# Performance work log

Measured on AMD Instinct MI355X. Metric: run time of the kernel, lower is better.

Reference implementation:

```python
import jax, jax.numpy as jnp
import numpy as np

B, C, H, W = 8, 512, 64, 64
NUMS, V_C = 1024, 512
RATE = 0.999


def _normalize(x):
    # matches torch F.normalize(dim=-1, eps=1e-12)
    return x / jnp.clip(jnp.linalg.norm(x, axis=-1, keepdims=True), 1e-12)


def setup_inputs() -> dict:
    key = jax.random.key(0)
    k1, k2, k3 = jax.random.split(key, 3)
    return {
        "x": jax.random.normal(k1, (B, C, H, W), dtype=jnp.float32),
        "noise_feature": jax.random.normal(k2, (NUMS, C), dtype=jnp.float32),
        "std": jax.random.normal(k3, (NUMS, V_C), dtype=jnp.float32),
    }


def reference(x, noise_feature, std):
    b, c, h, w = x.shape
    # (b,c,h,w) -> (n,c)
    xf = jnp.transpose(x, (0, 2, 3, 1)).reshape(-1, c)
    m = jax.lax.stop_gradient(noise_feature)  # torch uses .data (no grad)
    xn = _normalize(xf)
    mn = _normalize(m)
    score = xn @ mn.T  # (n, k) cosine similarities

    # EMA codebook update (training path, update_flag=True)
    xd = jax.lax.stop_gradient(xf)
    embed_ind = jnp.argmax(score, axis=1)  # (n,)
    # segment_sum == x.T @ one_hot(ind), transposed; avoids dense one-hot GEMM
    embed_sum = jax.ops.segment_sum(xd, embed_ind, num_segments=NUMS)  # (k, c)
    counts = jax.ops.segment_sum(jnp.ones((xd.shape[0],), xd.dtype), embed_ind,
                                 num_segments=NUMS)  # (k,)
    embed_mean = embed_sum / (counts[:, None] + 1e-6)
    new_m = m * RATE + embed_mean * (1.0 - RATE)

    mn2 = _normalize(new_m)
    score2 = xn @ mn2.T  # (n, k)
    soft_label = jax.nn.softmax(score2, axis=1)
    out = (soft_label @ std).reshape(b, h, w, V_C)
    return out, score2
```

## Files before the change

kernel.cpp:

```cpp
#include <hip/hip_runtime.h>
#include <stdint.h>

#define NROWS 32768
#define CDIM  512
#define KCODES 1024
#define VC    512

typedef unsigned short u16;
typedef unsigned long long u64;
using bf16x8 = __attribute__((ext_vector_type(8))) __bf16;
using f32x4  = __attribute__((ext_vector_type(4))) float;

__device__ __forceinline__ float bf2f(u16 u){
  union { unsigned int i; float f; } x; x.i = ((unsigned int)u) << 16; return x.f;
}
__device__ __forceinline__ u16 f2bf(float f){
  union { float f; unsigned int i; } x; x.f = f;
  unsigned int u = x.i;
  u += 0x7fffu + ((u >> 16) & 1u);
  return (u16)(u >> 16);
}
__device__ __forceinline__ unsigned int pack2(u16 lo, u16 hi){
  return (unsigned int)lo | ((unsigned int)hi << 16);
}
__device__ __forceinline__ unsigned int fkey(float f){
  unsigned int u = __float_as_uint(f);
  return (u & 0x80000000u) ? ~u : (u | 0x80000000u);
}
__device__ __forceinline__ f32x4 mfma16(bf16x8 a, bf16x8 b, f32x4 c){
  return __builtin_amdgcn_mfma_f32_16x16x32_bf16(a, b, c, 0, 0, 0);
}
__device__ __forceinline__ void gload_lds16(const void* g, void* l){
  __builtin_amdgcn_global_load_lds(
      (const __attribute__((address_space(1))) unsigned int*)g,
      (__attribute__((address_space(3))) unsigned int*)l, 16, 0, 0);
}

__global__ __launch_bounds__(256) void k_transpose_x(const float* __restrict__ x,
                                                     u16* __restrict__ xf){
  __shared__ float tile[32][33];
  int b  = blockIdx.z;
  int p0 = blockIdx.x * 32;
  int c0 = blockIdx.y * 32;
  int tx = threadIdx.x, ty = threadIdx.y;
  const float* xb = x + (size_t)b * CDIM * 4096;
#pragma unroll
  for (int i = 0; i < 4; i++){
    int c = c0 + ty + i * 8;
    tile[ty + i * 8][tx] = xb[(size_t)c * 4096 + p0 + tx];
  }
  __syncthreads();
#pragma unroll
  for (int i = 0; i < 4; i++){
    int p = p0 + ty + i * 8;
    xf[((size_t)(b * 4096 + p)) * CDIM + c0 + tx] = f2bf(tile[tx][ty + i * 8]);
  }
}

__global__ __launch_bounds__(256) void k_rownorm(const u16* __restrict__ xf,
                                                 float* __restrict__ rinv){
  int row  = blockIdx.x * 4 + (threadIdx.x >> 6);
  int lane = threadIdx.x & 63;
  const uint4* p = (const uint4*)(xf + (size_t)row * CDIM);
  uint4 v = p[lane];
  unsigned int w[4] = {v.x, v.y, v.z, v.w};
  float s = 0.f;
#pragma unroll
  for (int i = 0; i < 4; i++){
    float a = bf2f((u16)(w[i] & 0xffffu));
    float b = bf2f((u16)(w[i] >> 16));
    s += a * a + b * b;
  }
#pragma unroll
  for (int off = 32; off; off >>= 1) s += __shfl_xor(s, off, 64);
  if (lane == 0) rinv[row] = 1.0f / fmaxf(sqrtf(s), 1e-12f);
}

__global__ __launch_bounds__(256) void k_norm_rows(const float* __restrict__ in,
                                                   u16* __restrict__ out){
  int row  = blockIdx.x * 4 + (threadIdx.x >> 6);
  int lane = threadIdx.x & 63;
  const float* r = in + (size_t)row * CDIM;
  float v[8]; float s = 0.f;
#pragma unroll
  for (int i = 0; i < 8; i++){ v[i] = r[lane + i * 64]; s += v[i] * v[i]; }
#pragma unroll
  for (int off = 32; off; off >>= 1) s += __shfl_xor(s, off, 64);
  float inv = 1.0f / fmaxf(sqrtf(s), 1e-12f);
#pragma unroll
  for (int i = 0; i < 8; i++) out[(size_t)row * CDIM + lane + i * 64] = f2bf(v[i] * inv);
}

__global__ __launch_bounds__(256) void k_transpose_std(const float* __restrict__ sd,
                                                       u16* __restrict__ stdT){
  __shared__ float tile[32][33];
  int k0 = blockIdx.x * 32;
  int v0 = blockIdx.y * 32;
  int tx = threadIdx.x, ty = threadIdx.y;
#pragma unroll
  for (int i = 0; i < 4; i++)
    tile[ty + i * 8][tx] = sd[(size_t)(k0 + ty + i * 8) * VC + v0 + tx];
  __syncthreads();
#pragma unroll
  for (int i = 0; i < 4; i++)
    stdT[(size_t)(v0 + ty + i * 8) * KCODES + k0 + tx] = f2bf(tile[tx][ty + i * 8]);
}

__global__ __launch_bounds__(256) void k_gemm1_am(const u16* __restrict__ xf,
                                                  const u16* __restrict__ mn,
                                                  u64* __restrict__ packed){
  __shared__ u16 As[128 * 64];
  __shared__ u16 Bs[128 * 64];
  int tid  = threadIdx.x;
  int wave = tid >> 6, lane = tid & 63;
  int wr = wave >> 1, wc = wave & 1;
  int quad = lane >> 4, l15 = lane & 15;
  int c0 = blockIdx.x * 128, r0 = blockIdx.y * 128;

  int srow = lane >> 3, schunk = lane & 7;
  const u16* ag = xf + (size_t)(r0 + wave * 8 + srow) * CDIM + schunk * 8;
  const u16* bg = mn + (size_t)(c0 + wave * 8 + srow) * CDIM + schunk * 8;
  u16* adst = As + wave * 8 * 64;
  u16* bdst = Bs + wave * 8 * 64;

  f32x4 acc[4][4];
#pragma unroll
  for (int rt = 0; rt < 4; rt++)
#pragma unroll
    for (int ct = 0; ct < 4; ct++) acc[rt][ct] = (f32x4)(0.f);

  for (int k0 = 0; k0 < CDIM; k0 += 64){
#pragma unroll
    for (int i = 0; i < 4; i++){
      gload_lds16(ag + (size_t)i * 32 * CDIM + k0, adst + i * 32 * 64);
      gload_lds16(bg + (size_t)i * 32 * CDIM + k0, bdst + i * 32 * 64);
    }
    __syncthreads();
#pragma unroll
    for (int ks = 0; ks < 2; ks++){
      bf16x8 af[4], bfr[4];
#pragma unroll
      for (int rt = 0; rt < 4; rt++)
        af[rt] = *(const bf16x8*)(As + (wr * 64 + rt * 16 + l15) * 64 + ks * 32 + quad * 8);
#pragma unroll
      for (int ct = 0; ct < 4; ct++)
        bfr[ct] = *(const bf16x8*)(Bs + (wc * 64 + ct * 16 + l15) * 64 + ks * 32 + quad * 8);
#pragma unroll
      for (int rt = 0; rt < 4; rt++)
#pragma unroll
        for (int ct = 0; ct < 4; ct++)
          acc[rt][ct] = mfma16(af[rt], bfr[ct], acc[rt][ct]);
    }
    __syncthreads();
  }

#pragma unroll
  for (int rt = 0; rt < 4; rt++){
#pragma unroll
    for (int q = 0; q < 4; q++){
      float bv = acc[rt][0][q];
      int   bc = c0 + wc * 64 + l15;
#pragma unroll
      for (int ct = 1; ct < 4; ct++){
        float v = acc[rt][ct][q];
        int   c = c0 + wc * 64 + ct * 16 + l15;
        if (v > bv){ bv = v; bc = c; }
      }
#pragma unroll
      for (int off = 1; off <= 8; off <<= 1){
        float ov = __shfl_xor(bv, off, 64);
        int   oc = __shfl_xor(bc, off, 64);
        if (ov > bv || (ov == bv && oc < bc)){ bv = ov; bc = oc; }
      }
      if (l15 == 0){
        int rg = r0 + wr * 64 + rt * 16 + quad * 4 + q;
        u64 key = ((u64)fkey(bv) << 32) | (unsigned int)(~(unsigned int)bc);
        atomicMax(packed + rg, key);
      }
    }
  }
}

__global__ __launch_bounds__(256) void k_decode(const u64* __restrict__ packed,
                                                int* __restrict__ ind){
  int i = blockIdx.x * 256 + threadIdx.x;
  ind[i] = (int)(~(unsigned int)(packed[i] & 0xffffffffull)) & (KCODES - 1);
}

__global__ __launch_bounds__(256) void k_gather(const int* __restrict__ ind,
                                                const u16* __restrict__ xf,
                                                float* __restrict__ esum,
                                                float* __restrict__ counts){
  __shared__ float part[4][CDIM];
  __shared__ int   wcnt[4];
  int code = blockIdx.x;
  int tid = threadIdx.x, wave = tid >> 6, lane = tid & 63;
  float acc[8] = {0,0,0,0,0,0,0,0};
  int cnt = 0;
  for (int base = wave * 64; base < NROWS; base += 256){
    int match = (ind[base + lane] == code);
    u64 mask = __ballot(match);
    cnt += (int)__popcll(mask);
    while (mask){
      int b = __ffsll((long long)mask) - 1;
      mask &= mask - 1;
      int rr = base + b;
      uint4 v = *(const uint4*)(xf + (size_t)rr * CDIM + lane * 8);
      unsigned int w[4] = {v.x, v.y, v.z, v.w};
#pragma unroll
      for (int i = 0; i < 4; i++){
        acc[2 * i]     += bf2f((u16)(w[i] & 0xffffu));
        acc[2 * i + 1] += bf2f((u16)(w[i] >> 16));
      }
    }
  }
#pragma unroll
  for (int j = 0; j < 8; j++) part[wave][lane * 8 + j] = acc[j];
  if (lane == 0) wcnt[wave] = cnt;
  __syncthreads();
  for (int c = tid; c < CDIM; c += 256)
    esum[(size_t)code * CDIM + c] = part[0][c] + part[1][c] + part[2][c] + part[3][c];
  if (tid == 0) counts[code] = (float)(wcnt[0] + wcnt[1] + wcnt[2] + wcnt[3]);
}

__global__ __launch_bounds__(256) void k_newm(const float* __restrict__ m,
                                              const float* __restrict__ esum,
                                              const float* __restrict__ counts,
                                              u16* __restrict__ mn2){
  int row  = blockIdx.x * 4 + (threadIdx.x >> 6);
  int lane = threadIdx.x & 63;
  float cnt = counts[row];
  float sc  = 0.001f / (cnt + 1e-6f);
  float v[8]; float s = 0.f;
#pragma unroll
  for (int i = 0; i < 8; i++){
    int c = lane + i * 64;
    v[i] = m[(size_t)row * CDIM + c] * 0.999f + esum[(size_t)row * CDIM + c] * sc;
    s += v[i] * v[i];
  }
#pragma unroll
  for (int off = 32; off; off >>= 1) s += __shfl_xor(s, off, 64);
  float inv = 1.0f / fmaxf(sqrtf(s), 1e-12f);
#pragma unroll
  for (int i = 0; i < 8; i++) mn2[(size_t)row * CDIM + lane + i * 64] = f2bf(v[i] * inv);
}

#define SM_AS   0
#define SM_BS   65536
#define SM_VS   98304
#define SM_SF   131072
#define SM_PT   140288
#define SM_RM   144384
#define SM_RL   144640
#define SM_RS   144896
__global__ __launch_bounds__(512) void k_fused(const u16* __restrict__ xf,
                                               const u16* __restrict__ mn2,
                                               const float* __restrict__ rinv,
                                               const u16* __restrict__ stdT,
                                               float* __restrict__ score2,
                                               float* __restrict__ out){
  __shared__ char smem[145152];
  char* AsB = smem + SM_AS;
  char* BsB = smem + SM_BS;
  char* VsB = smem + SM_VS;
  float* Sf = (float*)(smem + SM_SF);
  char* PtB = smem + SM_PT;
  float* rowm = (float*)(smem + SM_RM);
  float* rowl = (float*)(smem + SM_RL);
  float* rowsc = (float*)(smem + SM_RS);

  int tid  = threadIdx.x;
  int wave = tid >> 6, lane = tid & 63;
  int quad = lane >> 4, l15 = lane & 15;
  int r0 = blockIdx.x * 64;

  int fr = wave >> 1, fc = wave & 1;
  int ar = fr * 16 + l15;
  int br = fc * 16 + l15;

  int wr2 = wave >> 2, wc4 = wave & 3;
  int R = wr2 * 32, C = wc4 * 128;

  int srow = tid >> 3, ssub = tid & 7;
  float rv = rinv[r0 + srow];

  f32x4 acc[2][8];
#pragma unroll
  for (int rt = 0; rt < 2; rt++)
#pragma unroll
    for (int ct = 0; ct < 8; ct++) acc[rt][ct] = (f32x4)(0.f);

#pragma unroll
  for (int i = 0; i < 8; i++){
    int rr = wave * 8 + i;
    gload_lds16(xf + (size_t)(r0 + rr) * CDIM + ((lane ^ (rr & 7)) * 8),
                AsB + rr * 1024);
  }
#pragma unroll
  for (int i = 0; i < 4; i++){
    int rr = wave + i * 8;
    gload_lds16(mn2 + (size_t)rr * CDIM + ((lane ^ (rr & 7)) * 8),
                BsB + rr * 1024);
  }
#pragma unroll
  for (int i = 0; i < 4; i++){
    int vb = (wave * 4 + i) * 16;
    int vc = vb + (lane >> 2);
    gload_lds16(stdT + (size_t)vc * KCODES + (((lane & 3) ^ (vc & 3)) * 8),
                VsB + vb * 64);
  }
  if (tid < 64){ rowm[tid] = -3.0e38f; rowl[tid] = 0.f; }
  asm volatile("s_waitcnt vmcnt(0)" ::: "memory");
  __syncthreads();

  for (int t = 0; t < 32; ++t){
    int kt = t * 32;
    f32x4 sacc = (f32x4)(0.f);
#pragma unroll
    for (int ks = 0; ks < 16; ++ks){
      bf16x8 a = *(const bf16x8*)(AsB + ar * 1024 + (((ks * 4 + quad) ^ (ar & 7)) << 4));
      bf16x8 b = *(const bf16x8*)(BsB + br * 1024 + (((ks * 4 + quad) ^ (br & 7)) << 4));
      sacc = mfma16(a, b, sacc);
    }
#pragma unroll
    for (int q = 0; q < 4; ++q)
      Sf[(fr * 16 + quad * 4 + q) * 36 + fc * 16 + l15] = sacc[q];
    asm volatile("s_waitcnt lgkmcnt(0)" ::: "memory");
    __builtin_amdgcn_s_barrier();
    if (t + 1 < 32){
#pragma unroll
      for (int i = 0; i < 4; i++){
        int rr = wave + i * 8;
        gload_lds16(mn2 + (size_t)(kt + 32 + rr) * CDIM + ((lane ^ (rr & 7)) * 8),
                    BsB + rr * 1024);
      }
    }
    {
      f32x4 v = *(const f32x4*)(Sf + srow * 36 + ssub * 4);
      v *= rv;
      *(f32x4*)(score2 + (size_t)(r0 + srow) * KCODES + kt + ssub * 4) = v;
      float mx = fmaxf(fmaxf(v[0], v[1]), fmaxf(v[2], v[3]));
      mx = fmaxf(mx, __shfl_xor(mx, 1, 64));
      mx = fmaxf(mx, __shfl_xor(mx, 2, 64));
      mx = fmaxf(mx, __shfl_xor(mx, 4, 64));
      float mo = rowm[srow];
      float mn_ = fmaxf(mo, mx);
      float d = __expf(mo - mn_);
      float p0 = __expf(v[0] - mn_), p1 = __expf(v[1] - mn_);
      float p2 = __expf(v[2] - mn_), p3 = __expf(v[3] - mn_);
      float ss = p0 + p1 + p2 + p3;
      ss += __shfl_xor(ss, 1, 64);
      ss += __shfl_xor(ss, 2, 64);
      ss += __shfl_xor(ss, 4, 64);
      if (ssub == 0){
        rowl[srow] = rowl[srow] * d + ss;
        rowm[srow] = mn_;
        rowsc[srow] = d;
      }
      uint2 pw;
      pw.x = pack2(f2bf(p0), f2bf(p1));
      pw.y = pack2(f2bf(p2), f2bf(p3));
      *(uint2*)(PtB + srow * 64 + (((ssub >> 1) ^ (srow & 3)) << 4) + ((ssub & 1) << 3)) = pw;
    }
    asm volatile("s_waitcnt vmcnt(4) lgkmcnt(0)" ::: "memory");
    __builtin_amdgcn_s_barrier();
    __builtin_amdgcn_sched_barrier(0);
#pragma unroll
    for (int rt = 0; rt < 2; rt++)
#pragma unroll
      for (int q = 0; q < 4; q++){
        float s = rowsc[R + rt * 16 + quad * 4 + q];
#pragma unroll
        for (int ct = 0; ct < 8; ct++) acc[rt][ct][q] *= s;
      }
    bf16x8 pa[2];
#pragma unroll
    for (int rt = 0; rt < 2; rt++){
      int rr = R + rt * 16 + l15;
      pa[rt] = *(const bf16x8*)(PtB + rr * 64 + ((quad ^ (rr & 3)) << 4));
    }
#pragma unroll
    for (int ct = 0; ct < 8; ct++){
      int vc = C + ct * 16 + l15;
      bf16x8 bv = *(const bf16x8*)(VsB + vc * 64 + ((quad ^ (vc & 3)) << 4));
#pragma unroll
      for (int rt = 0; rt < 2; rt++) acc[rt][ct] = mfma16(pa[rt], bv, acc[rt][ct]);
    }
    asm volatile("s_waitcnt lgkmcnt(0)" ::: "memory");
    __builtin_amdgcn_s_barrier();
    if (t + 1 < 32){
#pragma unroll
      for (int i = 0; i < 4; i++){
        int vb = (wave * 4 + i) * 16;
        int vc = vb + (lane >> 2);
        gload_lds16(stdT + (size_t)vc * KCODES + kt + 32 + (((lane & 3) ^ (vc & 3)) * 8),
                    VsB + vb * 64);
      }
      asm volatile("s_waitcnt vmcnt(4)" ::: "memory");
      __builtin_amdgcn_s_barrier();
      __builtin_amdgcn_sched_barrier(0);
    }
  }

#pragma unroll
  for (int rt = 0; rt < 2; rt++)
#pragma unroll
    for (int q = 0; q < 4; q++){
      int rr = R + rt * 16 + quad * 4 + q;
      float inv = 1.0f / rowl[rr];
#pragma unroll
      for (int ct = 0; ct < 8; ct++)
        out[(size_t)(r0 + rr) * VC + C + ct * 16 + l15] = acc[rt][ct][q] * inv;
    }
}

extern "C" void kernel_launch(void* const* d_in, const int* in_sizes, int n_in,
                              void* d_out, int out_size, void* d_ws, size_t ws_size,
                              hipStream_t stream){
  (void)in_sizes; (void)n_in; (void)out_size; (void)ws_size;
  const float* x      = (const float*)d_in[0];
  const float* m      = (const float*)d_in[1];
  const float* stdmat = (const float*)d_in[2];
  float* out    = (float*)d_out;
  float* score2 = out + (size_t)NROWS * VC;

  char* ws = (char*)d_ws;
  u16*   xf     = (u16*)  (ws + 0);
  u16*   mn     = (u16*)  (ws + 33554432);
  u16*   mn2    = (u16*)  (ws + 34603008);
  u16*   stdT   = (u16*)  (ws + 35651584);
  float* rinv   = (float*)(ws + 36700160);
  u64*   packed = (u64*)  (ws + 36831232);
  int*   ind    = (int*)  (ws + 37093376);
  float* esum   = (float*)(ws + 37224448);
  float* counts = (float*)(ws + 39321600);

  hipMemsetAsync(packed, 0, (size_t)NROWS * 8, stream);

  k_transpose_x  <<<dim3(128, 16, 8), dim3(32, 8), 0, stream>>>(x, xf);
  k_rownorm      <<<NROWS / 4, 256, 0, stream>>>(xf, rinv);
  k_norm_rows    <<<KCODES / 4, 256, 0, stream>>>(m, mn);
  k_transpose_std<<<dim3(32, 16), dim3(32, 8), 0, stream>>>(stdmat, stdT);
  k_gemm1_am     <<<dim3(KCODES / 128, NROWS / 128), 256, 0, stream>>>(xf, mn, packed);
  k_decode       <<<NROWS / 256, 256, 0, stream>>>(packed, ind);
  k_gather       <<<KCODES, 256, 0, stream>>>(ind, xf, esum, counts);
  k_newm         <<<KCODES / 4, 256, 0, stream>>>(m, esum, counts, mn2);
  k_fused        <<<NROWS / 64, 512, 0, stream>>>(xf, mn2, rinv, stdT, score2, out);
}
```

Measured before the change: 541.3 us.

## Enlarge code tile in fused softmax kernel and load std fragments directly

The fused score/softmax/output kernel now processes 64 codes per tile instead of 32, halving the number of online-softmax iterations and barriers. The std matrix is no longer staged through LDS; each wave reads its bf16 fragments straight from global memory into registers. Separately, the decode kernel is removed and the gather kernel decodes the packed argmax keys itself, saving one launch and an intermediate buffer. Direct global reads of std may expose memory latency that the earlier LDS prefetch hid, and the larger register footprint could lower occupancy.

```diff
diff --git a/kernel.cpp b/kernel.cpp
--- a/kernel.cpp
+++ b/kernel.cpp
@@ -109,8 +109,8 @@
 __global__ __launch_bounds__(256) void k_gemm1_am(const u16* __restrict__ xf,
                                                   const u16* __restrict__ mn,
                                                   u64* __restrict__ packed){
-  __shared__ u16 As[128 * 64];
-  __shared__ u16 Bs[128 * 64];
+  __shared__ __align__(16) u16 As[128 * 64];
+  __shared__ __align__(16) u16 Bs[128 * 64];
   int tid  = threadIdx.x;
   int wave = tid >> 6, lane = tid & 63;
   int wr = wave >> 1, wc = wave & 1;
@@ -181,13 +181,7 @@
   }
 }
 
-__global__ __launch_bounds__(256) void k_decode(const u64* __restrict__ packed,
-                                                int* __restrict__ ind){
-  int i = blockIdx.x * 256 + threadIdx.x;
-  ind[i] = (int)(~(unsigned int)(packed[i] & 0xffffffffull)) & (KCODES - 1);
-}
-
-__global__ __launch_bounds__(256) void k_gather(const int* __restrict__ ind,
+__global__ __launch_bounds__(256) void k_gather(const u64* __restrict__ packed,
                                                 const u16* __restrict__ xf,
                                                 float* __restrict__ esum,
                                                 float* __restrict__ counts){
@@ -198,7 +192,9 @@
   float acc[8] = {0,0,0,0,0,0,0,0};
   int cnt = 0;
   for (int base = wave * 64; base < NROWS; base += 256){
-    int match = (ind[base + lane] == code);
+    u64 pk = packed[base + lane];
+    int cl = (int)(~(unsigned int)(pk & 0xffffffffull)) & (KCODES - 1);
+    int match = (cl == code);
     u64 mask = __ballot(match);
     cnt += (int)__popcll(mask);
     while (mask){
@@ -245,41 +241,32 @@
   for (int i = 0; i < 8; i++) mn2[(size_t)row * CDIM + lane + i * 64] = f2bf(v[i] * inv);
 }
 
-#define SM_AS   0
-#define SM_BS   65536
-#define SM_VS   98304
-#define SM_SF   131072
-#define SM_PT   140288
-#define SM_RM   144384
-#define SM_RL   144640
-#define SM_RS   144896
+#define NTILE 16
+#define TCODE 64
 __global__ __launch_bounds__(512) void k_fused(const u16* __restrict__ xf,
                                                const u16* __restrict__ mn2,
                                                const float* __restrict__ rinv,
                                                const u16* __restrict__ stdT,
                                                float* __restrict__ score2,
                                                float* __restrict__ out){
-  __shared__ char smem[145152];
-  char* AsB = smem + SM_AS;
-  char* BsB = smem + SM_BS;
-  char* VsB = smem + SM_VS;
-  float* Sf = (float*)(smem + SM_SF);
-  char* PtB = smem + SM_PT;
-  float* rowm = (float*)(smem + SM_RM);
-  float* rowl = (float*)(smem + SM_RL);
-  float* rowsc = (float*)(smem + SM_RS);
+  __shared__ __align__(16) u16 As[64 * 512];
+  __shared__ __align__(16) u16 Bs[64 * 512];
+  __shared__ __align__(16) float Sf[64 * 68];
+  __shared__ __align__(16) u16 Pt[64 * 72];
+  __shared__ float rowm[64], rowl[64], rowsc[64];
 
   int tid  = threadIdx.x;
   int wave = tid >> 6, lane = tid & 63;
   int quad = lane >> 4, l15 = lane & 15;
   int r0 = blockIdx.x * 64;
 
-  int fr = wave >> 1, fc = wave & 1;
-  int ar = fr * 16 + l15;
-  int br = fc * 16 + l15;
-
-  int wr2 = wave >> 2, wc4 = wave & 3;
-  int R = wr2 * 32, C = wc4 * 128;
+  int sR = (wave >> 2) * 32;
+  int sC = (wave & 3) * 16;
+  int ar0 = sR + l15, ar1 = sR + 16 + l15;
+  int br  = sC + l15;
+
+  int R2 = (wave >> 2) * 32;
+  int C2 = (wave & 3) * 128;
 
   int srow = tid >> 3, ssub = tid & 7;
   float rv = rinv[r0 + srow];
@@ -294,61 +281,61 @@
   for (int i = 0; i < 8; i++){
     int rr = wave * 8 + i;
     gload_lds16(xf + (size_t)(r0 + rr) * CDIM + ((lane ^ (rr & 7)) * 8),
-                AsB + rr * 1024);
-  }
-#pragma unroll
-  for (int i = 0; i < 4; i++){
-    int rr = wave + i * 8;
+                As + rr * 512);
     gload_lds16(mn2 + (size_t)rr * CDIM + ((lane ^ (rr & 7)) * 8),
-                BsB + rr * 1024);
-  }
-#pragma unroll
-  for (int i = 0; i < 4; i++){
-    int vb = (wave * 4 + i) * 16;
-    int vc = vb + (lane >> 2);
-    gload_lds16(stdT + (size_t)vc * KCODES + (((lane & 3) ^ (vc & 3)) * 8),
-                VsB + vb * 64);
+                Bs + rr * 512);
   }
   if (tid < 64){ rowm[tid] = -3.0e38f; rowl[tid] = 0.f; }
   asm volatile("s_waitcnt vmcnt(0)" ::: "memory");
-  __syncthreads();
-
-  for (int t = 0; t < 32; ++t){
-    int kt = t * 32;
-    f32x4 sacc = (f32x4)(0.f);
+  __builtin_amdgcn_s_barrier();
+
+  for (int t = 0; t < NTILE; ++t){
+    int kt = t * TCODE;
+    f32x4 s0 = (f32x4)(0.f), s1 = (f32x4)(0.f);
 #pragma unroll
     for (int ks = 0; ks < 16; ++ks){
-      bf16x8 a = *(const bf16x8*)(AsB + ar * 1024 + (((ks * 4 + quad) ^ (ar & 7)) << 4));
-      bf16x8 b = *(const bf16x8*)(BsB + br * 1024 + (((ks * 4 + quad) ^ (br & 7)) << 4));
-      sacc = mfma16(a, b, sacc);
-    }
-#pragma unroll
-    for (int q = 0; q < 4; ++q)
-      Sf[(fr * 16 + quad * 4 + q) * 36 + fc * 16 + l15] = sacc[q];
+      bf16x8 b  = *(const bf16x8*)(Bs + br * 512 + (((ks * 4 + quad) ^ (br & 7)) << 3));
+      bf16x8 a0 = *(const bf16x8*)(As + ar0 * 512 + (((ks * 4 + quad) ^ (ar0 & 7)) << 3));
+      bf16x8 a1 = *(const bf16x8*)(As + ar1 * 512 + (((ks * 4 + quad) ^ (ar1 & 7)) << 3));
+      s0 = mfma16(a0, b, s0);
+      s1 = mfma16(a1, b, s1);
+    }
+#pragma unroll
+    for (int q = 0; q < 4; ++q){
+      Sf[(sR + quad * 4 + q) * 68 + sC + l15]      = s0[q];
+      Sf[(sR + 16 + quad * 4 + q) * 68 + sC + l15] = s1[q];
+    }
     asm volatile("s_waitcnt lgkmcnt(0)" ::: "memory");
     __builtin_amdgcn_s_barrier();
-    if (t + 1 < 32){
-#pragma unroll
-      for (int i = 0; i < 4; i++){
-        int rr = wave + i * 8;
-        gload_lds16(mn2 + (size_t)(kt + 32 + rr) * CDIM + ((lane ^ (rr & 7)) * 8),
-                    BsB + rr * 1024);
+    if (t + 1 < NTILE){
+#pragma unroll
+      for (int i = 0; i < 8; i++){
+        int rr = wave * 8 + i;
+        gload_lds16(mn2 + (size_t)(kt + TCODE + rr) * CDIM + ((lane ^ (rr & 7)) * 8),
+                    Bs + rr * 512);
       }
     }
     {
-      f32x4 v = *(const f32x4*)(Sf + srow * 36 + ssub * 4);
-      v *= rv;
-      *(f32x4*)(score2 + (size_t)(r0 + srow) * KCODES + kt + ssub * 4) = v;
-      float mx = fmaxf(fmaxf(v[0], v[1]), fmaxf(v[2], v[3]));
+      f32x4 u = *(const f32x4*)(Sf + srow * 68 + ssub * 8);
+      f32x4 w = *(const f32x4*)(Sf + srow * 68 + ssub * 8 + 4);
+      u *= rv; w *= rv;
+      float* so = score2 + (size_t)(r0 + srow) * KCODES + kt + ssub * 8;
+      *(f32x4*)(so)     = u;
+      *(f32x4*)(so + 4) = w;
+      float mx = fmaxf(fmaxf(fmaxf(u[0], u[1]), fmaxf(u[2], u[3])),
+                       fmaxf(fmaxf(w[0], w[1]), fmaxf(w[2], w[3])));
       mx = fmaxf(mx, __shfl_xor(mx, 1, 64));
       mx = fmaxf(mx, __shfl_xor(mx, 2, 64));
       mx = fmaxf(mx, __shfl_xor(mx, 4, 64));
       float mo = rowm[srow];
       float mn_ = fmaxf(mo, mx);
       float d = __expf(mo - mn_);
-      float p0 = __expf(v[0] - mn_), p1 = __expf(v[1] - mn_);
-      float p2 = __expf(v[2] - mn_), p3 = __expf(v[3] - mn_);
-      float ss = p0 + p1 + p2 + p3;
+      float p[8];
+#pragma unroll
+      for (int j = 0; j < 4; j++){ p[j] = __expf(u[j] - mn_); p[4 + j] = __expf(w[j] - mn_); }
+      float ss = 0.f;
+#pragma unroll
+      for (int j = 0; j < 8; j++) ss += p[j];
       ss += __shfl_xor(ss, 1, 64);
       ss += __shfl_xor(ss, 2, 64);
       ss += __shfl_xor(ss, 4, 64);
@@ -357,60 +344,58 @@
         rowm[srow] = mn_;
         rowsc[srow] = d;
       }
-      uint2 pw;
-      pw.x = pack2(f2bf(p0), f2bf(p1));
-      pw.y = pack2(f2bf(p2), f2bf(p3));
-      *(uint2*)(PtB + srow * 64 + (((ssub >> 1) ^ (srow & 3)) << 4) + ((ssub & 1) << 3)) = pw;
-    }
-    asm volatile("s_waitcnt vmcnt(4) lgkmcnt(0)" ::: "memory");
-    __builtin_amdgcn_s_barrier();
-    __builtin_amdgcn_sched_barrier(0);
-#pragma unroll
-    for (int rt = 0; rt < 2; rt++)
-#pragma unroll
-      for (int q = 0; q < 4; q++){
-        float s = rowsc[R + rt * 16 + quad * 4 + q];
-#pragma unroll
-        for (int ct = 0; ct < 8; ct++) acc[rt][ct][q] *= s;
-      }
-    bf16x8 pa[2];
-#pragma unroll
-    for (int rt = 0; rt < 2; rt++){
-      int rr = R + rt * 16 + l15;
-      pa[rt] = *(const bf16x8*)(PtB + rr * 64 + ((quad ^ (rr & 3)) << 4));
-    }
-#pragma unroll
-    for (int ct = 0; ct < 8; ct++){
-      int vc = C + ct * 16 + l15;
-      bf16x8 bv = *(const bf16x8*)(VsB + vc * 64 + ((quad ^ (vc & 3)) << 4));
-#pragma unroll
-      for (int rt = 0; rt < 2; rt++) acc[rt][ct] = mfma16(pa[rt], bv, acc[rt][ct]);
+      uint4 pw;
+      pw.x = pack2(f2bf(p[0]), f2bf(p[1]));
+      pw.y = pack2(f2bf(p[2]), f2bf(p[3]));
+      pw.z = pack2(f2bf(p[4]), f2bf(p[5]));
+      pw.w = pack2(f2bf(p[6]), f2bf(p[7]));
+      *(uint4*)(Pt + srow * 72 + ssub * 8) = pw;
     }
     asm volatile("s_waitcnt lgkmcnt(0)" ::: "memory");
     __builtin_amdgcn_s_barrier();
-    if (t + 1 < 32){
-#pragma unroll
-      for (int i = 0; i < 4; i++){
-        int vb = (wave * 4 + i) * 16;
-        int vc = vb + (lane >> 2);
-        gload_lds16(stdT + (size_t)vc * KCODES + kt + 32 + (((lane & 3) ^ (vc & 3)) * 8),
-                    VsB + vb * 64);
-      }
-      asm volatile("s_waitcnt vmcnt(4)" ::: "memory");
-      __builtin_amdgcn_s_barrier();
-      __builtin_amdgcn_sched_barrier(0);
-    }
+    bf16x8 vf[8][2];
+#pragma unroll
+    for (int ct = 0; ct < 8; ct++){
+      const u16* vp = stdT + (size_t)(C2 + ct * 16 + l15) * KCODES + kt + quad * 8;
+      vf[ct][0] = *(const bf16x8*)(vp);
+      vf[ct][1] = *(const bf16x8*)(vp + 32);
+    }
+#pragma unroll
+    for (int rt = 0; rt < 2; rt++)
+#pragma unroll
+      for (int q = 0; q < 4; q++){
+        float s = rowsc[R2 + rt * 16 + quad * 4 + q];
+#pragma unroll
+        for (int ct = 0; ct < 8; ct++) acc[rt][ct][q] *= s;
+      }
+    bf16x8 pa[2][2];
+#pragma unroll
+    for (int rt = 0; rt < 2; rt++){
+      int rr = R2 + rt * 16 + l15;
+#pragma unroll
+      for (int ks = 0; ks < 2; ks++)
+        pa[rt][ks] = *(const bf16x8*)(Pt + rr * 72 + (ks * 4 + quad) * 8);
+    }
+#pragma unroll
+    for (int ct = 0; ct < 8; ct++)
+#pragma unroll
+      for (int ks = 0; ks < 2; ks++)
+#pragma unroll
+        for (int rt = 0; rt < 2; rt++)
+          acc[rt][ct] = mfma16(pa[rt][ks], vf[ct][ks], acc[rt][ct]);
+    asm volatile("s_waitcnt vmcnt(0) lgkmcnt(0)" ::: "memory");
+    __builtin_amdgcn_s_barrier();
   }
 
 #pragma unroll
   for (int rt = 0; rt < 2; rt++)
 #pragma unroll
     for (int q = 0; q < 4; q++){
-      int rr = R + rt * 16 + quad * 4 + q;
+      int rr = R2 + rt * 16 + quad * 4 + q;
       float inv = 1.0f / rowl[rr];
 #pragma unroll
       for (int ct = 0; ct < 8; ct++)
-        out[(size_t)(r0 + rr) * VC + C + ct * 16 + l15] = acc[rt][ct][q] * inv;
+        out[(size_t)(r0 + rr) * VC + C2 + ct * 16 + l15] = acc[rt][ct][q] * inv;
     }
 }
 
@@ -431,7 +416,6 @@
   u16*   stdT   = (u16*)  (ws + 35651584);
   float* rinv   = (float*)(ws + 36700160);
   u64*   packed = (u64*)  (ws + 36831232);
-  int*   ind    = (int*)  (ws + 37093376);
   float* esum   = (float*)(ws + 37224448);
   float* counts = (float*)(ws + 39321600);
 
@@ -442,8 +426,7 @@
   k_norm_rows    <<<KCODES / 4, 256, 0, stream>>>(m, mn);
   k_transpose_std<<<dim3(32, 16), dim3(32, 8), 0, stream>>>(stdmat, stdT);
   k_gemm1_am     <<<dim3(KCODES / 128, NROWS / 128), 256, 0, stream>>>(xf, mn, packed);
-  k_decode       <<<NROWS / 256, 256, 0, stream>>>(packed, ind);
-  k_gather       <<<KCODES, 256, 0, stream>>>(ind, xf, esum, counts);
+  k_gather       <<<KCODES, 256, 0, stream>>>(packed, xf, esum, counts);
   k_newm         <<<KCODES / 4, 256, 0, stream>>>(m, esum, counts, mn2);
   k_fused        <<<NROWS / 64, 512, 0, stream>>>(xf, mn2, rinv, stdT, score2, out);
 }
```

Result: slower. 588.0 us (+8.6%).
